# Optimization experiments

Measured on AMD Instinct MI355X. Metric: run time of the kernel, lower is better.

## Reference

```python
import jax, jax.numpy as jnp
import numpy as np

B, N_IN, HID, N_OUT = 1024, 512, 64, 256


def setup_inputs() -> dict:
    key = jax.random.key(0)
    ks = jax.random.split(key, 10)
    s = 0.02
    return {
        "x": jax.random.normal(ks[0], (B, N_IN), dtype=jnp.float32),
        "ln_gamma": jnp.ones((N_IN,), dtype=jnp.float32),
        "ln_beta": jnp.zeros((N_IN,), dtype=jnp.float32),
        "Wq": jax.random.normal(ks[1], (N_IN, HID * N_OUT), dtype=jnp.float32) * s,
        "bq": jnp.zeros((HID * N_OUT,), dtype=jnp.float32),
        "Wk": jax.random.normal(ks[2], (N_IN, HID * N_OUT), dtype=jnp.float32) * s,
        "bk": jnp.zeros((HID * N_OUT,), dtype=jnp.float32),
        "Wv": jax.random.normal(ks[3], (N_IN, HID * N_OUT), dtype=jnp.float32) * s,
        "bv": jnp.zeros((HID * N_OUT,), dtype=jnp.float32),
        "Wo": jax.random.normal(ks[4], (HID, N_OUT), dtype=jnp.float32) * s,
        "bo": jnp.zeros((N_OUT,), dtype=jnp.float32),
    }


def reference(x, ln_gamma, ln_beta, Wq, bq, Wk, bk, Wv, bv, Wo, bo):
    # LayerNorm over last dim (input_shape)
    mu = jnp.mean(x, axis=-1, keepdims=True)
    var = jnp.mean(jnp.square(x - mu), axis=-1, keepdims=True)
    h = (x - mu) / jnp.sqrt(var + 1e-5) * ln_gamma + ln_beta  # (B, 512)

    # QKV projections, then view as (B, N_OUT, HID)
    q = (h @ Wq + bq).reshape(B, N_OUT, HID)
    k = (h @ Wk + bk).reshape(B, N_OUT, HID)
    v = (h @ Wv + bv).reshape(B, N_OUT, HID)

    # Single-head scaled dot-product attention over length N_OUT
    w = jnp.einsum("bqc,bkc->bqk", q, k) * (HID ** -0.5)
    w = jax.nn.softmax(w, axis=2)
    a = jnp.einsum("bqk,bkc->bqc", w, v)  # (B, N_OUT, HID)

    # Output projection, ReLU, negate -> seminegative contact map
    out = jax.nn.relu(a @ Wo + bo)  # (B, N_OUT, N_OUT)
    return -out
```

## Files before the change

kernel.cpp:

```cpp
#include <hip/hip_runtime.h>
#include <hip/hip_fp16.h>

typedef _Float16 h4_t __attribute__((ext_vector_type(4)));
typedef _Float16 h8_t __attribute__((ext_vector_type(8)));
typedef float f4_t __attribute__((ext_vector_type(4)));

#define B_SZ 1024
#define N_IN 512
#define HID 64
#define N_OUT 256
#define QKN (N_OUT * HID)

__global__ __launch_bounds__(256) void k_ln(const float* __restrict__ x,
                                            const float* __restrict__ gamma,
                                            const float* __restrict__ beta,
                                            _Float16* __restrict__ h16) {
    int tid = threadIdx.x;
    int wave = tid >> 6, lane = tid & 63;
    int row = blockIdx.x * 4 + wave;
    const float4* xr = (const float4*)(x + (size_t)row * N_IN);
    float4 a = xr[lane];
    float4 b = xr[lane + 64];
    float s = a.x + a.y + a.z + a.w + b.x + b.y + b.z + b.w;
    float sq = a.x * a.x + a.y * a.y + a.z * a.z + a.w * a.w +
               b.x * b.x + b.y * b.y + b.z * b.z + b.w * b.w;
    for (int off = 1; off < 64; off <<= 1) {
        s += __shfl_xor(s, off);
        sq += __shfl_xor(sq, off);
    }
    float mean = s * (1.0f / N_IN);
    float var = sq * (1.0f / N_IN) - mean * mean;
    float rstd = rsqrtf(var + 1e-5f);
    float4 g0 = ((const float4*)gamma)[lane];
    float4 g1 = ((const float4*)gamma)[lane + 64];
    float4 e0 = ((const float4*)beta)[lane];
    float4 e1 = ((const float4*)beta)[lane + 64];
    h4_t o0 = {(_Float16)((a.x - mean) * rstd * g0.x + e0.x),
               (_Float16)((a.y - mean) * rstd * g0.y + e0.y),
               (_Float16)((a.z - mean) * rstd * g0.z + e0.z),
               (_Float16)((a.w - mean) * rstd * g0.w + e0.w)};
    h4_t o1 = {(_Float16)((b.x - mean) * rstd * g1.x + e1.x),
               (_Float16)((b.y - mean) * rstd * g1.y + e1.y),
               (_Float16)((b.z - mean) * rstd * g1.z + e1.z),
               (_Float16)((b.w - mean) * rstd * g1.w + e1.w)};
    h4_t* hr = (h4_t*)(h16 + (size_t)row * N_IN);
    hr[lane] = o0;
    hr[lane + 64] = o1;
}

__global__ __launch_bounds__(256) void k_wt(const float* __restrict__ Wq,
                                            const float* __restrict__ Wk,
                                            const float* __restrict__ Wv,
                                            _Float16* __restrict__ wt) {
    __shared__ _Float16 t[64][65];
    const float* W = blockIdx.z == 0 ? Wq : (blockIdx.z == 1 ? Wk : Wv);
    _Float16* out = wt + (size_t)blockIdx.z * ((size_t)QKN * N_IN);
    int n0 = blockIdx.x * 64, k0 = blockIdx.y * 64;
    int c = threadIdx.x & 63, rq = threadIdx.x >> 6;
    for (int i = 0; i < 16; i++) {
        int r = i * 4 + rq;
        t[r][c] = (_Float16)W[(size_t)(k0 + r) * QKN + n0 + c];
    }
    __syncthreads();
    for (int i = 0; i < 16; i++) {
        int r = i * 4 + rq;
        out[(size_t)(n0 + r) * N_IN + k0 + c] = t[c][r];
    }
}

__global__ __launch_bounds__(256) void k_qkv(const _Float16* __restrict__ h16,
                                             const _Float16* __restrict__ wt,
                                             const float* __restrict__ bq,
                                             const float* __restrict__ bk,
                                             const float* __restrict__ bv,
                                             _Float16* __restrict__ qkv) {
    __shared__ _Float16 As[128 * 32];
    __shared__ _Float16 Bs[128 * 32];
    int z = blockIdx.z;
    const _Float16* Wb = wt + (size_t)z * ((size_t)QKN * N_IN);
    const float* bias = z == 0 ? bq : (z == 1 ? bk : bv);
    _Float16* out = qkv + (size_t)z * ((size_t)B_SZ * QKN);
    int m0 = blockIdx.x * 128, n0 = blockIdx.y * 128;
    int tid = threadIdx.x, lane = tid & 63, w = tid >> 6;
    int wm = w & 1, wn = w >> 1;
    int col16 = lane & 15, quad = lane >> 4;
    f4_t acc[4][4] = {};
    for (int kk = 0; kk < N_IN; kk += 32) {
        __syncthreads();
        for (int c = 0; c < 2; c++) {
            int idx = (w * 2 + c) * 512 + lane * 8;
            int row = idx >> 5, col = idx & 31;
            __builtin_amdgcn_global_load_lds(
                (const __attribute__((address_space(1))) void*)(h16 + (size_t)(m0 + row) * N_IN + kk + col),
                (__attribute__((address_space(3))) void*)(As + (w * 2 + c) * 512),
                16, 0, 0);
            __builtin_amdgcn_global_load_lds(
                (const __attribute__((address_space(1))) void*)(Wb + (size_t)(n0 + row) * N_IN + kk + col),
                (__attribute__((address_space(3))) void*)(Bs + (w * 2 + c) * 512),
                16, 0, 0);
        }
        __syncthreads();
        h8_t af[4], bf[4];
        for (int mt = 0; mt < 4; mt++)
            af[mt] = *(const h8_t*)(As + (wm * 64 + mt * 16 + col16) * 32 + quad * 8);
        for (int nt = 0; nt < 4; nt++)
            bf[nt] = *(const h8_t*)(Bs + (wn * 64 + nt * 16 + col16) * 32 + quad * 8);
        for (int mt = 0; mt < 4; mt++)
            for (int nt = 0; nt < 4; nt++)
                acc[mt][nt] = __builtin_amdgcn_mfma_f32_16x16x32_f16(af[mt], bf[nt], acc[mt][nt], 0, 0, 0);
    }
    for (int nt = 0; nt < 4; nt++) {
        int n = n0 + wn * 64 + nt * 16 + col16;
        float bb = bias[n];
        for (int mt = 0; mt < 4; mt++) {
            int mbase = m0 + wm * 64 + mt * 16 + quad * 4;
            for (int r = 0; r < 4; r++)
                out[(size_t)(mbase + r) * QKN + n] = (_Float16)(acc[mt][nt][r] + bb);
        }
    }
}

__global__ __launch_bounds__(256) void k_attn(const _Float16* __restrict__ qkv,
                                              const float* __restrict__ Wo,
                                              const float* __restrict__ bo,
                                              float* __restrict__ out) {
    __shared__ _Float16 lds[24576];
    int b = blockIdx.x;
    int tid = threadIdx.x, lane = tid & 63, w = tid >> 6;
    int col16 = lane & 15, quad = lane >> 4;
    const _Float16* qb = qkv + (size_t)b * QKN;
    const _Float16* kb = qkv + (size_t)(B_SZ + b) * QKN;
    const _Float16* vb = qkv + (size_t)(2 * B_SZ + b) * QKN;

    for (int r = 0; r < 8; r++) {
        int slab = r * 4 + w;
        int c8 = slab >> 2, kblk = slab & 3;
        __builtin_amdgcn_global_load_lds(
            (const __attribute__((address_space(1))) void*)(kb + (size_t)(kblk * 64 + lane) * 64 + c8 * 8),
            (__attribute__((address_space(3))) void*)(lds + slab * 512),
            16, 0, 0);
    }

    int kq = lane >> 2, k3 = lane & 3, kx = kq & 7;
    h8_t v0a = *(const h8_t*)(vb + (size_t)lane * 64 + w * 16);
    h8_t v0b = *(const h8_t*)(vb + (size_t)lane * 64 + w * 16 + 8);

    h8_t qf[4][2];
    int qbase = w * 64;
    for (int qt = 0; qt < 4; qt++)
        for (int ki = 0; ki < 2; ki++)
            qf[qt][ki] = *(const h8_t*)(qb + (size_t)(qbase + qt * 16 + col16) * 64 + ki * 32 + quad * 8);

    {
        _Float16* vp = lds + 16384 + kq * 256 + k3;
        for (int j = 0; j < 8; j++) vp[(size_t)((w * 16 + j) ^ kx) * 4] = v0a[j];
        for (int j = 0; j < 8; j++) vp[(size_t)((w * 16 + 8 + j) ^ kx) * 4] = v0b[j];
    }
    __syncthreads();

    f4_t o[4][4] = {};
    float mrun[4], lrun[4];
    for (int qt = 0; qt < 4; qt++) { mrun[qt] = -1e30f; lrun[qt] = 0.f; }
    const float sc = 0.125f * 1.44269504f;

    for (int chunk = 0; chunk < 4; chunk++) {
        int buf = chunk & 1;
        h8_t vna, vnb;
        if (chunk < 3) {
            vna = *(const h8_t*)(vb + (size_t)((chunk + 1) * 64 + lane) * 64 + w * 16);
            vnb = *(const h8_t*)(vb + (size_t)((chunk + 1) * 64 + lane) * 64 + w * 16 + 8);
        }
        for (int kc4 = 0; kc4 < 4; kc4++) {
            int kc = chunk * 4 + kc4;
            h8_t kf0 = *(const h8_t*)(lds + (size_t)(quad)*2048 + (size_t)(kc * 16 + col16) * 8);
            h8_t kf1 = *(const h8_t*)(lds + (size_t)(4 + quad) * 2048 + (size_t)(kc * 16 + col16) * 8);
            int kqr = kc4 * 4 + quad, kxr = kqr & 7;
            h4_t vf[4];
            for (int mt = 0; mt < 4; mt++)
                vf[mt] = *(const h4_t*)(lds + 16384 + buf * 4096 + kqr * 256 +
                                        (size_t)((mt * 16 + col16) ^ kxr) * 4);
            for (int qt = 0; qt < 4; qt++) {
                f4_t s = {};
                __builtin_amdgcn_s_setprio(1);
                s = __builtin_amdgcn_mfma_f32_16x16x32_f16(kf0, qf[qt][0], s, 0, 0, 0);
                s = __builtin_amdgcn_mfma_f32_16x16x32_f16(kf1, qf[qt][1], s, 0, 0, 0);
                __builtin_amdgcn_s_setprio(0);
                float cm = fmaxf(fmaxf(s[0], s[1]), fmaxf(s[2], s[3]));
                cm = fmaxf(cm, __shfl_xor(cm, 16));
                cm = fmaxf(cm, __shfl_xor(cm, 32));
                float m0 = mrun[qt];
                bool defer = __all(cm <= m0 + 44.0f) != 0;
                float mn = defer ? m0 : fmaxf(m0, cm);
                float msc = mn * sc;
                float p0 = exp2f(__builtin_fmaf(s[0], sc, -msc));
                float p1 = exp2f(__builtin_fmaf(s[1], sc, -msc));
                float p2 = exp2f(__builtin_fmaf(s[2], sc, -msc));
                float p3 = exp2f(__builtin_fmaf(s[3], sc, -msc));
                float ps = p0 + p1 + p2 + p3;
                ps += __shfl_xor(ps, 16);
                ps += __shfl_xor(ps, 32);
                if (defer) {
                    lrun[qt] += ps;
                } else {
                    float alpha = exp2f((m0 - mn) * sc);
                    lrun[qt] = lrun[qt] * alpha + ps;
                    mrun[qt] = mn;
                    for (int mt = 0; mt < 4; mt++) {
                        f4_t t = o[mt][qt];
                        t[0] *= alpha; t[1] *= alpha; t[2] *= alpha; t[3] *= alpha;
                        o[mt][qt] = t;
                    }
                }
                h4_t pf = {(_Float16)p0, (_Float16)p1, (_Float16)p2, (_Float16)p3};
                __builtin_amdgcn_s_setprio(1);
                for (int mt = 0; mt < 4; mt++)
                    o[mt][qt] = __builtin_amdgcn_mfma_f32_16x16x16f16(vf[mt], pf, o[mt][qt], 0, 0, 0);
                __builtin_amdgcn_s_setprio(0);
            }
        }
        if (chunk < 3) {
            _Float16* vp = lds + 16384 + (buf ^ 1) * 4096 + kq * 256 + k3;
            for (int j = 0; j < 8; j++) vp[(size_t)((w * 16 + j) ^ kx) * 4] = vna[j];
            for (int j = 0; j < 8; j++) vp[(size_t)((w * 16 + 8 + j) ^ kx) * 4] = vnb[j];
            __syncthreads();
        }
    }

    h4_t af[4][4];
    for (int qt = 0; qt < 4; qt++) {
        float rl = 1.0f / lrun[qt];
        for (int hk = 0; hk < 4; hk++) {
            f4_t t = o[hk][qt];
            af[qt][hk] = (h4_t){(_Float16)(t[0] * rl), (_Float16)(t[1] * rl),
                                (_Float16)(t[2] * rl), (_Float16)(t[3] * rl)};
        }
    }
    __syncthreads();
    for (int it = 0; it < 16; it++) {
        h4_t wv = {(_Float16)Wo[(size_t)(it * 4 + 0) * 256 + tid],
                   (_Float16)Wo[(size_t)(it * 4 + 1) * 256 + tid],
                   (_Float16)Wo[(size_t)(it * 4 + 2) * 256 + tid],
                   (_Float16)Wo[(size_t)(it * 4 + 3) * 256 + tid]};
        *(h4_t*)(lds + it * 1024 + tid * 4) = wv;
    }
    __syncthreads();

    float* outb = out + (size_t)b * (N_OUT * N_OUT);
    for (int nc = 0; nc < 4; nc++) {
        for (int nt = 0; nt < 4; nt++) {
            int no = nc * 64 + nt * 16 + col16;
            h4_t wf[4];
            for (int hk = 0; hk < 4; hk++)
                wf[hk] = *(const h4_t*)(lds + (hk * 4 + quad) * 1024 + no * 4);
            float bb = bo[no];
            for (int qt = 0; qt < 4; qt++) {
                f4_t a = {};
                __builtin_amdgcn_s_setprio(1);
                for (int hk = 0; hk < 4; hk++)
                    a = __builtin_amdgcn_mfma_f32_16x16x16f16(af[qt][hk], wf[hk], a, 0, 0, 0);
                __builtin_amdgcn_s_setprio(0);
                int qrow = qbase + qt * 16 + quad * 4;
                for (int r = 0; r < 4; r++) {
                    float v = a[r] + bb;
                    outb[(size_t)(qrow + r) * N_OUT + no] = (v > 0.f) ? -v : 0.f;
                }
            }
        }
    }
}

extern "C" void kernel_launch(void* const* d_in, const int* in_sizes, int n_in,
                              void* d_out, int out_size, void* d_ws, size_t ws_size,
                              hipStream_t stream) {
    const float* x = (const float*)d_in[0];
    const float* gamma = (const float*)d_in[1];
    const float* beta = (const float*)d_in[2];
    const float* Wq = (const float*)d_in[3];
    const float* bq = (const float*)d_in[4];
    const float* Wk = (const float*)d_in[5];
    const float* bk = (const float*)d_in[6];
    const float* Wv = (const float*)d_in[7];
    const float* bv = (const float*)d_in[8];
    const float* Wo = (const float*)d_in[9];
    const float* bo = (const float*)d_in[10];
    float* out = (float*)d_out;

    _Float16* h16 = (_Float16*)d_ws;
    _Float16* wt16 = h16 + (size_t)B_SZ * N_IN;
    _Float16* qkv16 = wt16 + (size_t)3 * QKN * N_IN;

    k_ln<<<dim3(B_SZ / 4), 256, 0, stream>>>(x, gamma, beta, h16);
    k_wt<<<dim3(QKN / 64, N_IN / 64, 3), 256, 0, stream>>>(Wq, Wk, Wv, wt16);
    k_qkv<<<dim3(B_SZ / 128, QKN / 128, 3), 256, 0, stream>>>(h16, wt16, bq, bk, bv, qkv16);
    k_attn<<<dim3(B_SZ), 256, 0, stream>>>(qkv16, Wo, bo, out);
}
```

Before: 586.8 us.

## Double-buffer QKV GEMM tiles, preload all V, vectorize output stores

The QKV GEMM now double-buffers its LDS tiles, so the next k-slice's global-to-LDS load is issued before the current slice's MFMAs, and the loop needs one barrier per step instead of two. The attention kernel loads all of V into a larger LDS region up front, removing the per-chunk V double buffer and its barriers, and drops the setprio hints. The output projection swaps MFMA operand order so each lane holds four consecutive output columns, allowing 16-byte vector stores and a vector bias load. The larger LDS footprint in both kernels may reduce occupancy.

```diff
diff --git a/kernel.cpp b/kernel.cpp
--- a/kernel.cpp
+++ b/kernel.cpp
@@ -74,8 +74,8 @@
                                              const float* __restrict__ bk,
                                              const float* __restrict__ bv,
                                              _Float16* __restrict__ qkv) {
-    __shared__ _Float16 As[128 * 32];
-    __shared__ _Float16 Bs[128 * 32];
+    __shared__ _Float16 As[2][4096];
+    __shared__ _Float16 Bs[2][4096];
     int z = blockIdx.z;
     const _Float16* Wb = wt + (size_t)z * ((size_t)QKN * N_IN);
     const float* bias = z == 0 ? bq : (z == 1 ? bk : bv);
@@ -84,31 +84,53 @@
     int tid = threadIdx.x, lane = tid & 63, w = tid >> 6;
     int wm = w & 1, wn = w >> 1;
     int col16 = lane & 15, quad = lane >> 4;
+
+    int idx0 = (w * 2 + 0) * 512 + lane * 8;
+    int idx1 = (w * 2 + 1) * 512 + lane * 8;
+    int row0 = idx0 >> 5, col0 = idx0 & 31;
+    int row1 = idx1 >> 5, col1 = idx1 & 31;
+    const _Float16* pa0 = h16 + (size_t)(m0 + row0) * N_IN + col0;
+    const _Float16* pa1 = h16 + (size_t)(m0 + row1) * N_IN + col1;
+    const _Float16* pb0 = Wb + (size_t)(n0 + row0) * N_IN + col0;
+    const _Float16* pb1 = Wb + (size_t)(n0 + row1) * N_IN + col1;
+
+#define STAGE_QKV(buf, kk)                                                          \
+    do {                                                                            \
+        __builtin_amdgcn_global_load_lds(                                           \
+            (const __attribute__((address_space(1))) void*)(pa0 + (kk)),            \
+            (__attribute__((address_space(3))) void*)(&As[buf][(w * 2 + 0) * 512]), \
+            16, 0, 0);                                                              \
+        __builtin_amdgcn_global_load_lds(                                           \
+            (const __attribute__((address_space(1))) void*)(pa1 + (kk)),            \
+            (__attribute__((address_space(3))) void*)(&As[buf][(w * 2 + 1) * 512]), \
+            16, 0, 0);                                                              \
+        __builtin_amdgcn_global_load_lds(                                           \
+            (const __attribute__((address_space(1))) void*)(pb0 + (kk)),            \
+            (__attribute__((address_space(3))) void*)(&Bs[buf][(w * 2 + 0) * 512]), \
+            16, 0, 0);                                                              \
+        __builtin_amdgcn_global_load_lds(                                           \
+            (const __attribute__((address_space(1))) void*)(pb1 + (kk)),            \
+            (__attribute__((address_space(3))) void*)(&Bs[buf][(w * 2 + 1) * 512]), \
+            16, 0, 0);                                                              \
+    } while (0)
+
     f4_t acc[4][4] = {};
-    for (int kk = 0; kk < N_IN; kk += 32) {
-        __syncthreads();
-        for (int c = 0; c < 2; c++) {
-            int idx = (w * 2 + c) * 512 + lane * 8;
-            int row = idx >> 5, col = idx & 31;
-            __builtin_amdgcn_global_load_lds(
-                (const __attribute__((address_space(1))) void*)(h16 + (size_t)(m0 + row) * N_IN + kk + col),
-                (__attribute__((address_space(3))) void*)(As + (w * 2 + c) * 512),
-                16, 0, 0);
-            __builtin_amdgcn_global_load_lds(
-                (const __attribute__((address_space(1))) void*)(Wb + (size_t)(n0 + row) * N_IN + kk + col),
-                (__attribute__((address_space(3))) void*)(Bs + (w * 2 + c) * 512),
-                16, 0, 0);
-        }
-        __syncthreads();
+    STAGE_QKV(0, 0);
+    __syncthreads();
+    for (int t = 0; t < 16; t++) {
+        int buf = t & 1;
+        if (t < 15) STAGE_QKV(buf ^ 1, (t + 1) * 32);
         h8_t af[4], bf[4];
         for (int mt = 0; mt < 4; mt++)
-            af[mt] = *(const h8_t*)(As + (wm * 64 + mt * 16 + col16) * 32 + quad * 8);
+            af[mt] = *(const h8_t*)(&As[buf][(wm * 64 + mt * 16 + col16) * 32 + quad * 8]);
         for (int nt = 0; nt < 4; nt++)
-            bf[nt] = *(const h8_t*)(Bs + (wn * 64 + nt * 16 + col16) * 32 + quad * 8);
+            bf[nt] = *(const h8_t*)(&Bs[buf][(wn * 64 + nt * 16 + col16) * 32 + quad * 8]);
         for (int mt = 0; mt < 4; mt++)
             for (int nt = 0; nt < 4; nt++)
                 acc[mt][nt] = __builtin_amdgcn_mfma_f32_16x16x32_f16(af[mt], bf[nt], acc[mt][nt], 0, 0, 0);
-    }
+        __syncthreads();
+    }
+#undef STAGE_QKV
     for (int nt = 0; nt < 4; nt++) {
         int n = n0 + wn * 64 + nt * 16 + col16;
         float bb = bias[n];
@@ -124,7 +146,7 @@
                                               const float* __restrict__ Wo,
                                               const float* __restrict__ bo,
                                               float* __restrict__ out) {
-    __shared__ _Float16 lds[24576];
+    __shared__ _Float16 lds[32768];
     int b = blockIdx.x;
     int tid = threadIdx.x, lane = tid & 63, w = tid >> 6;
     int col16 = lane & 15, quad = lane >> 4;
@@ -141,9 +163,16 @@
             16, 0, 0);
     }
 
-    int kq = lane >> 2, k3 = lane & 3, kx = kq & 7;
-    h8_t v0a = *(const h8_t*)(vb + (size_t)lane * 64 + w * 16);
-    h8_t v0b = *(const h8_t*)(vb + (size_t)lane * 64 + w * 16 + 8);
+    int kq_ = lane >> 2, k3 = lane & 3;
+    for (int kc = 0; kc < 4; kc++) {
+        h8_t va = *(const h8_t*)(vb + (size_t)(kc * 64 + lane) * 64 + w * 16);
+        h8_t vc = *(const h8_t*)(vb + (size_t)(kc * 64 + lane) * 64 + w * 16 + 8);
+        int kq = kc * 16 + kq_;
+        int kx = kq & 7;
+        _Float16* vp = lds + 16384 + kq * 256 + k3;
+        for (int j = 0; j < 8; j++) vp[(size_t)((w * 16 + j) ^ kx) * 4] = va[j];
+        for (int j = 0; j < 8; j++) vp[(size_t)((w * 16 + 8 + j) ^ kx) * 4] = vc[j];
+    }
 
     h8_t qf[4][2];
     int qbase = w * 64;
@@ -151,11 +180,6 @@
         for (int ki = 0; ki < 2; ki++)
             qf[qt][ki] = *(const h8_t*)(qb + (size_t)(qbase + qt * 16 + col16) * 64 + ki * 32 + quad * 8);
 
-    {
-        _Float16* vp = lds + 16384 + kq * 256 + k3;
-        for (int j = 0; j < 8; j++) vp[(size_t)((w * 16 + j) ^ kx) * 4] = v0a[j];
-        for (int j = 0; j < 8; j++) vp[(size_t)((w * 16 + 8 + j) ^ kx) * 4] = v0b[j];
-    }
     __syncthreads();
 
     f4_t o[4][4] = {};
@@ -163,66 +187,47 @@
     for (int qt = 0; qt < 4; qt++) { mrun[qt] = -1e30f; lrun[qt] = 0.f; }
     const float sc = 0.125f * 1.44269504f;
 
-    for (int chunk = 0; chunk < 4; chunk++) {
-        int buf = chunk & 1;
-        h8_t vna, vnb;
-        if (chunk < 3) {
-            vna = *(const h8_t*)(vb + (size_t)((chunk + 1) * 64 + lane) * 64 + w * 16);
-            vnb = *(const h8_t*)(vb + (size_t)((chunk + 1) * 64 + lane) * 64 + w * 16 + 8);
-        }
-        for (int kc4 = 0; kc4 < 4; kc4++) {
-            int kc = chunk * 4 + kc4;
-            h8_t kf0 = *(const h8_t*)(lds + (size_t)(quad)*2048 + (size_t)(kc * 16 + col16) * 8);
-            h8_t kf1 = *(const h8_t*)(lds + (size_t)(4 + quad) * 2048 + (size_t)(kc * 16 + col16) * 8);
-            int kqr = kc4 * 4 + quad, kxr = kqr & 7;
-            h4_t vf[4];
+    for (int kc = 0; kc < 16; kc++) {
+        h8_t kf0 = *(const h8_t*)(lds + (size_t)quad * 2048 + (size_t)(kc * 16 + col16) * 8);
+        h8_t kf1 = *(const h8_t*)(lds + (size_t)(4 + quad) * 2048 + (size_t)(kc * 16 + col16) * 8);
+        int kqr = kc * 4 + quad, kxr = kqr & 7;
+        h4_t vf[4];
+        for (int mt = 0; mt < 4; mt++)
+            vf[mt] = *(const h4_t*)(lds + 16384 + kqr * 256 +
+                                    (size_t)((mt * 16 + col16) ^ kxr) * 4);
+        for (int qt = 0; qt < 4; qt++) {
+            f4_t s = {};
+            s = __builtin_amdgcn_mfma_f32_16x16x32_f16(kf0, qf[qt][0], s, 0, 0, 0);
+            s = __builtin_amdgcn_mfma_f32_16x16x32_f16(kf1, qf[qt][1], s, 0, 0, 0);
+            float cm = fmaxf(fmaxf(s[0], s[1]), fmaxf(s[2], s[3]));
+            cm = fmaxf(cm, __shfl_xor(cm, 16));
+            cm = fmaxf(cm, __shfl_xor(cm, 32));
+            float m0v = mrun[qt];
+            bool defer = __all(cm <= m0v + 44.0f) != 0;
+            float mn = defer ? m0v : fmaxf(m0v, cm);
+            float msc = mn * sc;
+            float p0 = exp2f(__builtin_fmaf(s[0], sc, -msc));
+            float p1 = exp2f(__builtin_fmaf(s[1], sc, -msc));
+            float p2 = exp2f(__builtin_fmaf(s[2], sc, -msc));
+            float p3 = exp2f(__builtin_fmaf(s[3], sc, -msc));
+            float ps = p0 + p1 + p2 + p3;
+            ps += __shfl_xor(ps, 16);
+            ps += __shfl_xor(ps, 32);
+            if (defer) {
+                lrun[qt] += ps;
+            } else {
+                float alpha = exp2f((m0v - mn) * sc);
+                lrun[qt] = lrun[qt] * alpha + ps;
+                mrun[qt] = mn;
+                for (int mt = 0; mt < 4; mt++) {
+                    f4_t t = o[mt][qt];
+                    t[0] *= alpha; t[1] *= alpha; t[2] *= alpha; t[3] *= alpha;
+                    o[mt][qt] = t;
+                }
+            }
+            h4_t pf = {(_Float16)p0, (_Float16)p1, (_Float16)p2, (_Float16)p3};
             for (int mt = 0; mt < 4; mt++)
-                vf[mt] = *(const h4_t*)(lds + 16384 + buf * 4096 + kqr * 256 +
-                                        (size_t)((mt * 16 + col16) ^ kxr) * 4);
-            for (int qt = 0; qt < 4; qt++) {
-                f4_t s = {};
-                __builtin_amdgcn_s_setprio(1);
-                s = __builtin_amdgcn_mfma_f32_16x16x32_f16(kf0, qf[qt][0], s, 0, 0, 0);
-                s = __builtin_amdgcn_mfma_f32_16x16x32_f16(kf1, qf[qt][1], s, 0, 0, 0);
-                __builtin_amdgcn_s_setprio(0);
-                float cm = fmaxf(fmaxf(s[0], s[1]), fmaxf(s[2], s[3]));
-                cm = fmaxf(cm, __shfl_xor(cm, 16));
-                cm = fmaxf(cm, __shfl_xor(cm, 32));
-                float m0 = mrun[qt];
-                bool defer = __all(cm <= m0 + 44.0f) != 0;
-                float mn = defer ? m0 : fmaxf(m0, cm);
-                float msc = mn * sc;
-                float p0 = exp2f(__builtin_fmaf(s[0], sc, -msc));
-                float p1 = exp2f(__builtin_fmaf(s[1], sc, -msc));
-                float p2 = exp2f(__builtin_fmaf(s[2], sc, -msc));
-                float p3 = exp2f(__builtin_fmaf(s[3], sc, -msc));
-                float ps = p0 + p1 + p2 + p3;
-                ps += __shfl_xor(ps, 16);
-                ps += __shfl_xor(ps, 32);
-                if (defer) {
-                    lrun[qt] += ps;
-                } else {
-                    float alpha = exp2f((m0 - mn) * sc);
-                    lrun[qt] = lrun[qt] * alpha + ps;
-                    mrun[qt] = mn;
-                    for (int mt = 0; mt < 4; mt++) {
-                        f4_t t = o[mt][qt];
-                        t[0] *= alpha; t[1] *= alpha; t[2] *= alpha; t[3] *= alpha;
-                        o[mt][qt] = t;
-                    }
-                }
-                h4_t pf = {(_Float16)p0, (_Float16)p1, (_Float16)p2, (_Float16)p3};
-                __builtin_amdgcn_s_setprio(1);
-                for (int mt = 0; mt < 4; mt++)
-                    o[mt][qt] = __builtin_amdgcn_mfma_f32_16x16x16f16(vf[mt], pf, o[mt][qt], 0, 0, 0);
-                __builtin_amdgcn_s_setprio(0);
-            }
-        }
-        if (chunk < 3) {
-            _Float16* vp = lds + 16384 + (buf ^ 1) * 4096 + kq * 256 + k3;
-            for (int j = 0; j < 8; j++) vp[(size_t)((w * 16 + j) ^ kx) * 4] = vna[j];
-            for (int j = 0; j < 8; j++) vp[(size_t)((w * 16 + 8 + j) ^ kx) * 4] = vnb[j];
-            __syncthreads();
+                o[mt][qt] = __builtin_amdgcn_mfma_f32_16x16x16f16(vf[mt], pf, o[mt][qt], 0, 0, 0);
         }
     }
 
@@ -252,18 +257,19 @@
             h4_t wf[4];
             for (int hk = 0; hk < 4; hk++)
                 wf[hk] = *(const h4_t*)(lds + (hk * 4 + quad) * 1024 + no * 4);
-            float bb = bo[no];
+            f4_t bb = *(const f4_t*)(bo + nc * 64 + nt * 16 + quad * 4);
             for (int qt = 0; qt < 4; qt++) {
                 f4_t a = {};
-                __builtin_amdgcn_s_setprio(1);
                 for (int hk = 0; hk < 4; hk++)
-                    a = __builtin_amdgcn_mfma_f32_16x16x16f16(af[qt][hk], wf[hk], a, 0, 0, 0);
-                __builtin_amdgcn_s_setprio(0);
-                int qrow = qbase + qt * 16 + quad * 4;
+                    a = __builtin_amdgcn_mfma_f32_16x16x16f16(wf[hk], af[qt][hk], a, 0, 0, 0);
+                int q = qbase + qt * 16 + col16;
+                int nob = nc * 64 + nt * 16 + quad * 4;
+                f4_t v;
                 for (int r = 0; r < 4; r++) {
-                    float v = a[r] + bb;
-                    outb[(size_t)(qrow + r) * N_OUT + no] = (v > 0.f) ? -v : 0.f;
+                    float t = a[r] + bb[r];
+                    v[r] = (t > 0.f) ? -t : 0.f;
                 }
+                *(f4_t*)(outb + (size_t)q * N_OUT + nob) = v;
             }
         }
     }
```

After: 530.2 us. 1.11x faster.
